# Kernel optimization log

Measured on AMD Instinct MI355X. Metric: run time of the kernel, lower is better.

Reference implementation:

```python
import jax, jax.numpy as jnp
import numpy as np

HEADS = 8
DIM_HEAD = 64
SCALE = DIM_HEAD ** (-0.5)


def setup_inputs() -> dict:
    key = jax.random.key(0)
    k1, k2, k3 = jax.random.split(key, 3)
    b, dim, w = 8, 256, 2048
    hidden = HEADS * DIM_HEAD  # 512
    x = jax.random.normal(k1, (b, dim, w), dtype=jnp.float32)
    # Conv1d kernel-size-1 weights collapse to matrices; scale like torch init
    w_qkv = jax.random.normal(k2, (3 * hidden, dim), dtype=jnp.float32) * (1.0 / np.sqrt(dim))
    w_out = jax.random.normal(k3, (dim, hidden), dtype=jnp.float32) * (1.0 / np.sqrt(hidden))
    b_out = jnp.zeros((dim,), dtype=jnp.float32)
    return {"x": x, "w_qkv": w_qkv, "w_out": w_out, "b_out": b_out}


def reference(x, w_qkv, w_out, b_out):
    b, c, w = x.shape
    h, dh = HEADS, DIM_HEAD
    # 1x1 conv == matmul over channel dim: [3*hidden, dim] x [b, dim, w] -> [b, 3*hidden, w]
    qkv = jnp.einsum('od,bdw->bow', w_qkv, x)
    q, k, v = jnp.split(qkv, 3, axis=1)
    # 'b (h c) x -> b h c x'
    q = q.reshape(b, h, dh, w) * SCALE
    k = k.reshape(b, h, dh, w)
    v = v.reshape(b, h, dh, w)
    sim = jnp.einsum('bhdi,bhdj->bhij', q, k)          # [b, h, w, w]
    sim = sim - jax.lax.stop_gradient(sim.max(axis=-1, keepdims=True))
    attn = jax.nn.softmax(sim, axis=-1)
    out = jnp.einsum('bhij,bhdj->bhid', attn, v)        # [b, h, w, dh]
    # 'b h x c -> b (h c) x'
    out = out.transpose(0, 1, 3, 2).reshape(b, h * dh, w)
    # output 1x1 conv with bias
    return jnp.einsum('oc,bcw->bow', w_out, out) + b_out[None, :, None]
```

## Files before the change

### kernel.cpp

```cpp
#include <hip/hip_runtime.h>
#include <hip/hip_bf16.h>

typedef __bf16 bf16x8 __attribute__((ext_vector_type(8)));
typedef float f32x4 __attribute__((ext_vector_type(4)));
typedef float f32x16 __attribute__((ext_vector_type(16)));
typedef unsigned u32x4 __attribute__((ext_vector_type(4)));

#define MFMA16x16(a, b, c) __builtin_amdgcn_mfma_f32_16x16x32_bf16((a), (b), (c), 0, 0, 0)
#define MFMA32x32(a, b, c) __builtin_amdgcn_mfma_f32_32x32x16_bf16((a), (b), (c), 0, 0, 0)

namespace {
constexpr int BATCH = 8;
constexpr int DIMC  = 256;
constexpr int WLEN  = 2048;
constexpr int DH    = 64;
constexpr int HID   = 512;
constexpr float QSCALE = 0.125f * 1.44269504088896340736f;

constexpr size_t OFF_WQKV = 0;
constexpr size_t OFF_WOUT = 786432;
constexpr size_t OFF_XT   = 1048576;
constexpr size_t OFF_QKT  = 9437184;
constexpr size_t OFF_V    = 42991616;
constexpr size_t OFF_AT   = 59768832;
}

__device__ inline unsigned cvt_pk_bf16(float a, float b) {
  unsigned r;
  asm("v_cvt_pk_bf16_f32 %0, %1, %2" : "=v"(r) : "v"(a), "v"(b));
  return r;
}

__device__ inline void permswap(unsigned &a, unsigned &b) {
  asm("v_permlane32_swap_b32 %0, %1" : "+v"(a), "+v"(b));
}

__device__ inline u32x4 gload16(const void* p) {
  u32x4 r;
  asm volatile("global_load_dwordx4 %0, %1, off" : "=v"(r) : "v"(p));
  return r;
}
__device__ inline void vmwait0() {
  asm volatile("s_waitcnt vmcnt(0)" ::: "memory");
  __builtin_amdgcn_sched_barrier(0);
}

union U4 { unsigned u[4]; bf16x8 v; };

__device__ inline float softmax_half(const f32x16 st, bf16x8 &pfa, bf16x8 &pfb) {
  float e[16];
#pragma unroll
  for (int r = 0; r < 16; ++r) e[r] = __builtin_amdgcn_exp2f(st[r]);
  float t0 = (e[0] + e[1]) + (e[2] + e[3]);
  float t1 = (e[4] + e[5]) + (e[6] + e[7]);
  float t2 = (e[8] + e[9]) + (e[10] + e[11]);
  float t3 = (e[12] + e[13]) + (e[14] + e[15]);
  float rs = (t0 + t1) + (t2 + t3);
  unsigned w[8];
#pragma unroll
  for (int q = 0; q < 8; ++q) w[q] = cvt_pk_bf16(e[2 * q], e[2 * q + 1]);
  unsigned a0 = w[0], a1 = w[1], a2 = w[2], a3 = w[3];
  permswap(a0, a2);
  permswap(a1, a3);
  U4 ua; ua.u[0] = a0; ua.u[1] = a1; ua.u[2] = a2; ua.u[3] = a3;
  pfa = ua.v;
  unsigned b0 = w[4], b1 = w[5], b2 = w[6], b3 = w[7];
  permswap(b0, b2);
  permswap(b1, b3);
  U4 ub; ub.u[0] = b0; ub.u[1] = b1; ub.u[2] = b2; ub.u[3] = b3;
  pfb = ub.v;
  return rs;
}

__global__ __launch_bounds__(256) void prep_weights(
    const float* __restrict__ wqkv, const float* __restrict__ wout,
    __hip_bfloat16* __restrict__ wqkv_bf, __hip_bfloat16* __restrict__ wout_bf) {
  int i = blockIdx.x * 256 + threadIdx.x;
  if (i < 1536 * 256) wqkv_bf[i] = __float2bfloat16(wqkv[i]);
  if (i < 256 * 512)  wout_bf[i] = __float2bfloat16(wout[i]);
}

__global__ __launch_bounds__(256) void transpose_x(
    const float* __restrict__ x, __hip_bfloat16* __restrict__ xT) {
  __shared__ float t[64][65];
  int b = blockIdx.z;
  int d0 = blockIdx.y * 64, w0 = blockIdx.x * 64;
  int tid = threadIdx.x;
  const float* xb = x + (size_t)b * DIMC * WLEN;
#pragma unroll
  for (int r = 0; r < 16; ++r) {
    int dd = r * 4 + (tid >> 6);
    int ww = tid & 63;
    t[dd][ww] = xb[(size_t)(d0 + dd) * WLEN + w0 + ww];
  }
  __syncthreads();
  __hip_bfloat16* xTb = xT + (size_t)b * WLEN * DIMC;
#pragma unroll
  for (int r = 0; r < 16; ++r) {
    int ww = r * 4 + (tid >> 6);
    int dd = tid & 63;
    xTb[(size_t)(w0 + ww) * DIMC + d0 + dd] = __float2bfloat16(t[dd][ww]);
  }
}

__global__ __launch_bounds__(256) void qkv_gemm(
    const __hip_bfloat16* __restrict__ wqkv_bf,
    const __hip_bfloat16* __restrict__ xT,
    __hip_bfloat16* __restrict__ qkT, __hip_bfloat16* __restrict__ vbuf) {
  int b = blockIdx.z;
  int o0 = blockIdx.y * 128, w0 = blockIdx.x * 128;
  int tid = threadIdx.x;
  int wid = tid >> 6, lane = tid & 63;
  int il = lane & 31, hi = lane >> 5;
  int wo = (wid >> 1) * 64;
  int ww = (wid & 1) * 64;

  __shared__ __align__(16) char lds_raw[36864];
  __hip_bfloat16* Al = reinterpret_cast<__hip_bfloat16*>(lds_raw);
  __hip_bfloat16* Bl = Al + 2 * 128 * 36;

  const __hip_bfloat16* xb = xT + (size_t)b * WLEN * DIMC;

  const int srow = tid >> 2;
  const int scol = (tid & 3) * 8;
  const __hip_bfloat16* asrc = wqkv_bf + (size_t)(o0 + srow) * DIMC + scol;
  const __hip_bfloat16* bsrc = xb + (size_t)(w0 + srow) * DIMC + scol;

  u32x4 ga0, ga1, gb0, gb1;
  auto stage_load = [&](int k0) {
    ga0 = gload16(asrc + k0);
    ga1 = gload16(asrc + 64 * DIMC + k0);
    gb0 = gload16(bsrc + k0);
    gb1 = gload16(bsrc + 64 * DIMC + k0);
  };
  auto stage_write = [&](int bf) {
    vmwait0();
    *reinterpret_cast<u32x4*>(Al + (bf * 128 + srow) * 36 + scol)      = ga0;
    *reinterpret_cast<u32x4*>(Al + (bf * 128 + srow + 64) * 36 + scol) = ga1;
    *reinterpret_cast<u32x4*>(Bl + (bf * 128 + srow) * 36 + scol)      = gb0;
    *reinterpret_cast<u32x4*>(Bl + (bf * 128 + srow + 64) * 36 + scol) = gb1;
  };

  f32x16 acc[2][2];
#pragma unroll
  for (int ta = 0; ta < 2; ++ta)
#pragma unroll
    for (int tb = 0; tb < 2; ++tb)
#pragma unroll
      for (int r = 0; r < 16; ++r) acc[ta][tb][r] = 0.f;

  auto compute = [&](int cur) {
    bf16x8 af[2][2], bfr[2][2];
#pragma unroll
    for (int ta = 0; ta < 2; ++ta)
#pragma unroll
      for (int kk = 0; kk < 2; ++kk) {
        af[ta][kk] = *reinterpret_cast<const bf16x8*>(
            Al + (cur * 128 + wo + ta * 32 + il) * 36 + kk * 16 + hi * 8);
        bfr[ta][kk] = *reinterpret_cast<const bf16x8*>(
            Bl + (cur * 128 + ww + ta * 32 + il) * 36 + kk * 16 + hi * 8);
      }
    __builtin_amdgcn_s_setprio(1);
#pragma unroll
    for (int kk = 0; kk < 2; ++kk)
#pragma unroll
      for (int ta = 0; ta < 2; ++ta)
#pragma unroll
        for (int tb = 0; tb < 2; ++tb)
          acc[ta][tb] = MFMA32x32(af[ta][kk], bfr[tb][kk], acc[ta][tb]);
    __builtin_amdgcn_s_setprio(0);
  };

  stage_load(0);
  stage_write(0);
  __syncthreads();
#pragma unroll 1
  for (int t = 0; t < 7; ++t) {
    stage_load((t + 1) * 32);
    compute(t & 1);
    stage_write((t + 1) & 1);
    __syncthreads();
  }
  compute(1);
  __syncthreads();

  if (o0 < 1024) {
    float scale = (o0 < 512) ? QSCALE : 1.0f;
    __hip_bfloat16* bw = reinterpret_cast<__hip_bfloat16*>(lds_raw);
#pragma unroll
    for (int ta = 0; ta < 2; ++ta)
#pragma unroll
      for (int tb = 0; tb < 2; ++tb)
#pragma unroll
        for (int q = 0; q < 8; ++q) {
          int dl = ((2 * q) & 3) + 8 * (q >> 1) + 4 * hi;
          int row = ww + tb * 32 + il;
          int col = wo + ta * 32 + dl;
          unsigned pk = cvt_pk_bf16(acc[ta][tb][2 * q] * scale,
                                    acc[ta][tb][2 * q + 1] * scale);
          *reinterpret_cast<unsigned*>(bw + row * 136 + col) = pk;
        }
    __syncthreads();
    __hip_bfloat16* outq = qkT + (size_t)b * WLEN * 1024;
#pragma unroll
    for (int it = 0; it < 8; ++it) {
      int row = it * 16 + (tid >> 4);
      int c = (tid & 15) * 8;
      bf16x8 v = *reinterpret_cast<const bf16x8*>(bw + row * 136 + c);
      *reinterpret_cast<bf16x8*>(outq + (size_t)(w0 + row) * 1024 + o0 + c) = v;
    }
  } else {
    __hip_bfloat16* bo = reinterpret_cast<__hip_bfloat16*>(lds_raw);
#pragma unroll
    for (int ta = 0; ta < 2; ++ta)
#pragma unroll
      for (int tb = 0; tb < 2; ++tb)
#pragma unroll
        for (int r = 0; r < 16; ++r) {
          int orow = wo + ta * 32 + (r & 3) + 8 * (r >> 2) + 4 * hi;
          int wcol = ww + tb * 32 + il;
          bo[orow * 136 + wcol] = __float2bfloat16(acc[ta][tb][r]);
        }
    __syncthreads();
    __hip_bfloat16* outv = vbuf + (size_t)b * HID * WLEN;
#pragma unroll
    for (int it = 0; it < 8; ++it) {
      int orow = it * 16 + (tid >> 4);
      int c = (tid & 15) * 8;
      bf16x8 v = *reinterpret_cast<const bf16x8*>(bo + orow * 136 + c);
      *reinterpret_cast<bf16x8*>(outv + (size_t)(o0 - 1024 + orow) * WLEN + w0 + c) = v;
    }
  }
}

__global__ __launch_bounds__(256) void attn_kernel(
    const __hip_bfloat16* __restrict__ qkT,
    const __hip_bfloat16* __restrict__ vbuf,
    __hip_bfloat16* __restrict__ attnT) {
  int f = blockIdx.x;
  int xcd = f & 7, slot = f >> 3;
  int b = slot >> 4;
  int h = xcd;
  int xb = slot & 15;
  int tid = threadIdx.x, wid = tid >> 6, lane = tid & 63;
  int il = lane & 31, hi = lane >> 5;
  int i0w = xb * 128 + wid * 32;

  const __hip_bfloat16* qk_b = qkT + (size_t)b * WLEN * 1024;
  const __hip_bfloat16* vb = vbuf + (size_t)b * HID * WLEN + (size_t)h * DH * WLEN;

  __shared__ __align__(16) __hip_bfloat16 Kl[2][64][72];
  __shared__ __align__(16) __hip_bfloat16 Vl[2][64][72];

  bf16x8 qf[4];
  {
    const __hip_bfloat16* qrow = qk_b + (size_t)(i0w + il) * 1024 + h * 64 + hi * 8;
#pragma unroll
    for (int s = 0; s < 4; ++s)
      qf[s] = *reinterpret_cast<const bf16x8*>(qrow + s * 16);
  }

  f32x16 oacc0, oacc1;
#pragma unroll
  for (int r = 0; r < 16; ++r) { oacc0[r] = 0.f; oacc1[r] = 0.f; }
  float l_lane = 0.f;

  const int srow = tid >> 3;
  const int scol = (tid & 7) * 8;
  const __hip_bfloat16* ksrc = qk_b + 512 + h * 64 + scol;
  const __hip_bfloat16* vsrc = vb + scol;

  u32x4 gk0, gk1, gv0, gv1;
  auto stage_load = [&](int j0) {
    gk0 = gload16(ksrc + (size_t)(j0 + srow) * 1024);
    gk1 = gload16(ksrc + (size_t)(j0 + srow + 32) * 1024);
    gv0 = gload16(vsrc + (size_t)srow * WLEN + j0);
    gv1 = gload16(vsrc + (size_t)(srow + 32) * WLEN + j0);
  };
  auto stage_write = [&](int bf) {
    vmwait0();
    *reinterpret_cast<u32x4*>(&Kl[bf][srow][scol])      = gk0;
    *reinterpret_cast<u32x4*>(&Kl[bf][srow + 32][scol]) = gk1;
    *reinterpret_cast<u32x4*>(&Vl[bf][srow][scol])      = gv0;
    *reinterpret_cast<u32x4*>(&Vl[bf][srow + 32][scol]) = gv1;
  };

  auto compute = [&](int cur) {
    f32x16 st0, st1;
#pragma unroll
    for (int r = 0; r < 16; ++r) { st0[r] = 0.f; st1[r] = 0.f; }
    __builtin_amdgcn_s_setprio(1);
#pragma unroll
    for (int s = 0; s < 4; ++s)
      st0 = MFMA32x32(*reinterpret_cast<const bf16x8*>(&Kl[cur][il][s * 16 + hi * 8]),
                      qf[s], st0);
#pragma unroll
    for (int s = 0; s < 4; ++s)
      st1 = MFMA32x32(*reinterpret_cast<const bf16x8*>(&Kl[cur][il + 32][s * 16 + hi * 8]),
                      qf[s], st1);
    __builtin_amdgcn_s_setprio(0);

    bf16x8 p0, p1, p2, p3;
    l_lane += softmax_half(st0, p0, p1);
    l_lane += softmax_half(st1, p2, p3);

    __builtin_amdgcn_s_setprio(1);
    oacc0 = MFMA32x32(*reinterpret_cast<const bf16x8*>(&Vl[cur][il][hi * 8]),      p0, oacc0);
    oacc1 = MFMA32x32(*reinterpret_cast<const bf16x8*>(&Vl[cur][il + 32][hi * 8]), p0, oacc1);
    oacc0 = MFMA32x32(*reinterpret_cast<const bf16x8*>(&Vl[cur][il][16 + hi * 8]),      p1, oacc0);
    oacc1 = MFMA32x32(*reinterpret_cast<const bf16x8*>(&Vl[cur][il + 32][16 + hi * 8]), p1, oacc1);
    oacc0 = MFMA32x32(*reinterpret_cast<const bf16x8*>(&Vl[cur][il][32 + hi * 8]),      p2, oacc0);
    oacc1 = MFMA32x32(*reinterpret_cast<const bf16x8*>(&Vl[cur][il + 32][32 + hi * 8]), p2, oacc1);
    oacc0 = MFMA32x32(*reinterpret_cast<const bf16x8*>(&Vl[cur][il][48 + hi * 8]),      p3, oacc0);
    oacc1 = MFMA32x32(*reinterpret_cast<const bf16x8*>(&Vl[cur][il + 32][48 + hi * 8]), p3, oacc1);
    __builtin_amdgcn_s_setprio(0);
  };

  stage_load(0);
  stage_write(0);
  __syncthreads();

  constexpr int NT = WLEN / 64;
#pragma unroll 1
  for (int t = 0; t < NT - 1; ++t) {
    stage_load((t + 1) * 64);
    compute(t & 1);
    stage_write((t + 1) & 1);
    __syncthreads();
  }
  compute((NT - 1) & 1);
  __syncthreads();

  float l = l_lane + __shfl_xor(l_lane, 32);
  __hip_bfloat16* olds = &Kl[0][0][0];
  float rl = 1.0f / l;
#pragma unroll
  for (int q = 0; q < 8; ++q) {
    int dl = ((2 * q) & 3) + 8 * (q >> 1) + 4 * hi;
    unsigned pk0 = cvt_pk_bf16(oacc0[2 * q] * rl, oacc0[2 * q + 1] * rl);
    unsigned pk1 = cvt_pk_bf16(oacc1[2 * q] * rl, oacc1[2 * q + 1] * rl);
    *reinterpret_cast<unsigned*>(olds + (wid * 32 + il) * 72 + dl)      = pk0;
    *reinterpret_cast<unsigned*>(olds + (wid * 32 + il) * 72 + 32 + dl) = pk1;
  }
  __hip_bfloat16* ob = attnT + (size_t)b * WLEN * HID + h * 64;
  int dcol = (lane & 7) * 8;
#pragma unroll
  for (int it = 0; it < 4; ++it) {
    int ir = it * 8 + (lane >> 3);
    bf16x8 vrow = *reinterpret_cast<const bf16x8*>(olds + (wid * 32 + ir) * 72 + dcol);
    *reinterpret_cast<bf16x8*>(ob + (size_t)(i0w + ir) * HID + dcol) = vrow;
  }
}

__global__ __launch_bounds__(256) void out_proj(
    const __hip_bfloat16* __restrict__ attnT,
    const __hip_bfloat16* __restrict__ wout_bf,
    const float* __restrict__ b_out, float* __restrict__ out) {
  int b = blockIdx.z;
  int o0 = blockIdx.y * 128, w0 = blockIdx.x * 64;
  int tid = threadIdx.x;
  int wid = tid >> 6, lane = tid & 63;
  int il = lane & 31, hi = lane >> 5;
  int wo = (wid >> 1) * 64;
  int ww = (wid & 1) * 32;

  __shared__ __align__(16) __hip_bfloat16 Al[2][128][36];
  __shared__ __align__(16) __hip_bfloat16 Bl[2][64][36];

  const __hip_bfloat16* at_b = attnT + (size_t)b * WLEN * HID;

  const int srow = tid >> 2;
  const int scol = (tid & 3) * 8;
  const __hip_bfloat16* asrc = wout_bf + (size_t)(o0 + srow) * HID + scol;
  const __hip_bfloat16* bsrc = at_b + (size_t)(w0 + srow) * HID + scol;

  u32x4 ga0, ga1, gb0;
  auto stage_load = [&](int k0) {
    ga0 = gload16(asrc + k0);
    ga1 = gload16(asrc + 64 * HID + k0);
    gb0 = gload16(bsrc + k0);
  };
  auto stage_write = [&](int bf) {
    vmwait0();
    *reinterpret_cast<u32x4*>(&Al[bf][srow][scol])      = ga0;
    *reinterpret_cast<u32x4*>(&Al[bf][srow + 64][scol]) = ga1;
    *reinterpret_cast<u32x4*>(&Bl[bf][srow][scol])      = gb0;
  };

  f32x16 acc[2];
#pragma unroll
  for (int ta = 0; ta < 2; ++ta)
#pragma unroll
    for (int r = 0; r < 16; ++r) acc[ta][r] = 0.f;

  auto compute = [&](int cur) {
    bf16x8 af[2][2], bfr[2];
#pragma unroll
    for (int kk = 0; kk < 2; ++kk) {
      bfr[kk] = *reinterpret_cast<const bf16x8*>(&Bl[cur][ww + il][kk * 16 + hi * 8]);
#pragma unroll
      for (int ta = 0; ta < 2; ++ta)
        af[ta][kk] = *reinterpret_cast<const bf16x8*>(
            &Al[cur][wo + ta * 32 + il][kk * 16 + hi * 8]);
    }
    __builtin_amdgcn_s_setprio(1);
#pragma unroll
    for (int kk = 0; kk < 2; ++kk)
#pragma unroll
      for (int ta = 0; ta < 2; ++ta)
        acc[ta] = MFMA32x32(af[ta][kk], bfr[kk], acc[ta]);
    __builtin_amdgcn_s_setprio(0);
  };

  stage_load(0);
  stage_write(0);
  __syncthreads();
#pragma unroll 1
  for (int t = 0; t < 15; ++t) {
    stage_load((t + 1) * 32);
    compute(t & 1);
    stage_write((t + 1) & 1);
    __syncthreads();
  }
  compute(1);

  float* outb = out + (size_t)b * DIMC * WLEN;
#pragma unroll
  for (int ta = 0; ta < 2; ++ta)
#pragma unroll
    for (int r = 0; r < 16; ++r) {
      int og = o0 + wo + ta * 32 + (r & 3) + 8 * (r >> 2) + 4 * hi;
      int wg = w0 + ww + il;
      outb[(size_t)og * WLEN + wg] = acc[ta][r] + b_out[og];
    }
}

extern "C" void kernel_launch(void* const* d_in, const int* in_sizes, int n_in,
                              void* d_out, int out_size, void* d_ws, size_t ws_size,
                              hipStream_t stream) {
  const float* x    = (const float*)d_in[0];
  const float* wqkv = (const float*)d_in[1];
  const float* wout = (const float*)d_in[2];
  const float* bout = (const float*)d_in[3];
  float* out = (float*)d_out;
  char* ws = (char*)d_ws;

  __hip_bfloat16* wqkv_bf = (__hip_bfloat16*)(ws + OFF_WQKV);
  __hip_bfloat16* wout_bf = (__hip_bfloat16*)(ws + OFF_WOUT);
  __hip_bfloat16* xT      = (__hip_bfloat16*)(ws + OFF_XT);
  __hip_bfloat16* qkT     = (__hip_bfloat16*)(ws + OFF_QKT);
  __hip_bfloat16* vbuf    = (__hip_bfloat16*)(ws + OFF_V);
  __hip_bfloat16* attnT   = (__hip_bfloat16*)(ws + OFF_AT);

  prep_weights<<<dim3(1536), dim3(256), 0, stream>>>(wqkv, wout, wqkv_bf, wout_bf);
  transpose_x<<<dim3(WLEN / 64, DIMC / 64, BATCH), dim3(256), 0, stream>>>(x, xT);
  qkv_gemm<<<dim3(WLEN / 128, 1536 / 128, BATCH), dim3(256), 0, stream>>>(wqkv_bf, xT, qkT, vbuf);
  attn_kernel<<<dim3(1024), dim3(256), 0, stream>>>(qkT, vbuf, attnT);
  out_proj<<<dim3(WLEN / 64, DIMC / 128, BATCH), dim3(256), 0, stream>>>(attnT, wout_bf, bout, out);
}
```

Before: 190.7 us.

## Process 64 query rows per wave in attention to reuse K/V fragments

Each wave now handles two 32-row query tiles (A and B), so every K and V fragment read from LDS feeds four MFMAs instead of two. The grid is halved to 512 blocks of 256 query rows each. Shared memory becomes a padded raw 72KB buffer, which limits occupancy to about two blocks per CU. The goal is to cut LDS traffic and K/V global loads per unit of work, at the cost of higher register pressure and fewer blocks to spread across the CUs.

```diff
diff --git a/kernel.cpp b/kernel.cpp
--- a/kernel.cpp
+++ b/kernel.cpp
@@ -238,32 +238,37 @@
     const __hip_bfloat16* __restrict__ vbuf,
     __hip_bfloat16* __restrict__ attnT) {
   int f = blockIdx.x;
-  int xcd = f & 7, slot = f >> 3;
-  int b = slot >> 4;
-  int h = xcd;
-  int xb = slot & 15;
+  int h = f & 7, slot = f >> 3;
+  int b = slot >> 3;
+  int xb = slot & 7;
   int tid = threadIdx.x, wid = tid >> 6, lane = tid & 63;
   int il = lane & 31, hi = lane >> 5;
-  int i0w = xb * 128 + wid * 32;
+  int i0w = xb * 256 + wid * 64;
 
   const __hip_bfloat16* qk_b = qkT + (size_t)b * WLEN * 1024;
   const __hip_bfloat16* vb = vbuf + (size_t)b * HID * WLEN + (size_t)h * DH * WLEN;
 
-  __shared__ __align__(16) __hip_bfloat16 Kl[2][64][72];
-  __shared__ __align__(16) __hip_bfloat16 Vl[2][64][72];
-
-  bf16x8 qf[4];
+  __shared__ __align__(16) char araw[73728];
+  __hip_bfloat16* Kl = reinterpret_cast<__hip_bfloat16*>(araw);
+  __hip_bfloat16* Vl = Kl + 2 * 64 * 72;
+
+  bf16x8 qfA[4], qfB[4];
   {
-    const __hip_bfloat16* qrow = qk_b + (size_t)(i0w + il) * 1024 + h * 64 + hi * 8;
-#pragma unroll
-    for (int s = 0; s < 4; ++s)
-      qf[s] = *reinterpret_cast<const bf16x8*>(qrow + s * 16);
-  }
-
-  f32x16 oacc0, oacc1;
-#pragma unroll
-  for (int r = 0; r < 16; ++r) { oacc0[r] = 0.f; oacc1[r] = 0.f; }
-  float l_lane = 0.f;
+    const __hip_bfloat16* qa = qk_b + (size_t)(i0w + il) * 1024 + h * 64 + hi * 8;
+#pragma unroll
+    for (int s = 0; s < 4; ++s) {
+      qfA[s] = *reinterpret_cast<const bf16x8*>(qa + s * 16);
+      qfB[s] = *reinterpret_cast<const bf16x8*>(qa + 32 * 1024 + s * 16);
+    }
+  }
+
+  f32x16 oA0, oA1, oB0, oB1;
+  f32x16 fzero;
+#pragma unroll
+  for (int r = 0; r < 16; ++r) {
+    oA0[r] = 0.f; oA1[r] = 0.f; oB0[r] = 0.f; oB1[r] = 0.f; fzero[r] = 0.f;
+  }
+  float lA = 0.f, lB = 0.f;
 
   const int srow = tid >> 3;
   const int scol = (tid & 7) * 8;
@@ -279,40 +284,52 @@
   };
   auto stage_write = [&](int bf) {
     vmwait0();
-    *reinterpret_cast<u32x4*>(&Kl[bf][srow][scol])      = gk0;
-    *reinterpret_cast<u32x4*>(&Kl[bf][srow + 32][scol]) = gk1;
-    *reinterpret_cast<u32x4*>(&Vl[bf][srow][scol])      = gv0;
-    *reinterpret_cast<u32x4*>(&Vl[bf][srow + 32][scol]) = gv1;
+    *reinterpret_cast<u32x4*>(Kl + (bf * 64 + srow) * 72 + scol)      = gk0;
+    *reinterpret_cast<u32x4*>(Kl + (bf * 64 + srow + 32) * 72 + scol) = gk1;
+    *reinterpret_cast<u32x4*>(Vl + (bf * 64 + srow) * 72 + scol)      = gv0;
+    *reinterpret_cast<u32x4*>(Vl + (bf * 64 + srow + 32) * 72 + scol) = gv1;
   };
 
   auto compute = [&](int cur) {
-    f32x16 st0, st1;
-#pragma unroll
-    for (int r = 0; r < 16; ++r) { st0[r] = 0.f; st1[r] = 0.f; }
+    f32x16 sA0, sA1, sB0, sB1;
+    const __hip_bfloat16* kb = Kl + (size_t)cur * 64 * 72 + hi * 8;
     __builtin_amdgcn_s_setprio(1);
-#pragma unroll
-    for (int s = 0; s < 4; ++s)
-      st0 = MFMA32x32(*reinterpret_cast<const bf16x8*>(&Kl[cur][il][s * 16 + hi * 8]),
-                      qf[s], st0);
-#pragma unroll
-    for (int s = 0; s < 4; ++s)
-      st1 = MFMA32x32(*reinterpret_cast<const bf16x8*>(&Kl[cur][il + 32][s * 16 + hi * 8]),
-                      qf[s], st1);
+    {
+      bf16x8 k0 = *reinterpret_cast<const bf16x8*>(kb + il * 72);
+      bf16x8 k1 = *reinterpret_cast<const bf16x8*>(kb + (il + 32) * 72);
+      sA0 = MFMA32x32(k0, qfA[0], fzero);
+      sA1 = MFMA32x32(k1, qfA[0], fzero);
+      sB0 = MFMA32x32(k0, qfB[0], fzero);
+      sB1 = MFMA32x32(k1, qfB[0], fzero);
+    }
+#pragma unroll
+    for (int s = 1; s < 4; ++s) {
+      bf16x8 k0 = *reinterpret_cast<const bf16x8*>(kb + il * 72 + s * 16);
+      bf16x8 k1 = *reinterpret_cast<const bf16x8*>(kb + (il + 32) * 72 + s * 16);
+      sA0 = MFMA32x32(k0, qfA[s], sA0);
+      sA1 = MFMA32x32(k1, qfA[s], sA1);
+      sB0 = MFMA32x32(k0, qfB[s], sB0);
+      sB1 = MFMA32x32(k1, qfB[s], sB1);
+    }
     __builtin_amdgcn_s_setprio(0);
 
-    bf16x8 p0, p1, p2, p3;
-    l_lane += softmax_half(st0, p0, p1);
-    l_lane += softmax_half(st1, p2, p3);
-
+    bf16x8 pA[4], pB[4];
+    lA += softmax_half(sA0, pA[0], pA[1]);
+    lA += softmax_half(sA1, pA[2], pA[3]);
+    lB += softmax_half(sB0, pB[0], pB[1]);
+    lB += softmax_half(sB1, pB[2], pB[3]);
+
+    const __hip_bfloat16* vbl = Vl + (size_t)cur * 64 * 72 + hi * 8;
     __builtin_amdgcn_s_setprio(1);
-    oacc0 = MFMA32x32(*reinterpret_cast<const bf16x8*>(&Vl[cur][il][hi * 8]),      p0, oacc0);
-    oacc1 = MFMA32x32(*reinterpret_cast<const bf16x8*>(&Vl[cur][il + 32][hi * 8]), p0, oacc1);
-    oacc0 = MFMA32x32(*reinterpret_cast<const bf16x8*>(&Vl[cur][il][16 + hi * 8]),      p1, oacc0);
-    oacc1 = MFMA32x32(*reinterpret_cast<const bf16x8*>(&Vl[cur][il + 32][16 + hi * 8]), p1, oacc1);
-    oacc0 = MFMA32x32(*reinterpret_cast<const bf16x8*>(&Vl[cur][il][32 + hi * 8]),      p2, oacc0);
-    oacc1 = MFMA32x32(*reinterpret_cast<const bf16x8*>(&Vl[cur][il + 32][32 + hi * 8]), p2, oacc1);
-    oacc0 = MFMA32x32(*reinterpret_cast<const bf16x8*>(&Vl[cur][il][48 + hi * 8]),      p3, oacc0);
-    oacc1 = MFMA32x32(*reinterpret_cast<const bf16x8*>(&Vl[cur][il + 32][48 + hi * 8]), p3, oacc1);
+#pragma unroll
+    for (int ks = 0; ks < 4; ++ks) {
+      bf16x8 v0 = *reinterpret_cast<const bf16x8*>(vbl + il * 72 + ks * 16);
+      bf16x8 v1 = *reinterpret_cast<const bf16x8*>(vbl + (il + 32) * 72 + ks * 16);
+      oA0 = MFMA32x32(v0, pA[ks], oA0);
+      oA1 = MFMA32x32(v1, pA[ks], oA1);
+      oB0 = MFMA32x32(v0, pB[ks], oB0);
+      oB1 = MFMA32x32(v1, pB[ks], oB1);
+    }
     __builtin_amdgcn_s_setprio(0);
   };
 
@@ -331,24 +348,30 @@
   compute((NT - 1) & 1);
   __syncthreads();
 
-  float l = l_lane + __shfl_xor(l_lane, 32);
-  __hip_bfloat16* olds = &Kl[0][0][0];
-  float rl = 1.0f / l;
+  lA += __shfl_xor(lA, 32);
+  lB += __shfl_xor(lB, 32);
+  float rlA = 1.0f / lA, rlB = 1.0f / lB;
+  __hip_bfloat16* olds = reinterpret_cast<__hip_bfloat16*>(araw);
+  int rowA = wid * 64 + il, rowB = rowA + 32;
 #pragma unroll
   for (int q = 0; q < 8; ++q) {
     int dl = ((2 * q) & 3) + 8 * (q >> 1) + 4 * hi;
-    unsigned pk0 = cvt_pk_bf16(oacc0[2 * q] * rl, oacc0[2 * q + 1] * rl);
-    unsigned pk1 = cvt_pk_bf16(oacc1[2 * q] * rl, oacc1[2 * q + 1] * rl);
-    *reinterpret_cast<unsigned*>(olds + (wid * 32 + il) * 72 + dl)      = pk0;
-    *reinterpret_cast<unsigned*>(olds + (wid * 32 + il) * 72 + 32 + dl) = pk1;
+    *reinterpret_cast<unsigned*>(olds + rowA * 72 + dl) =
+        cvt_pk_bf16(oA0[2 * q] * rlA, oA0[2 * q + 1] * rlA);
+    *reinterpret_cast<unsigned*>(olds + rowA * 72 + 32 + dl) =
+        cvt_pk_bf16(oA1[2 * q] * rlA, oA1[2 * q + 1] * rlA);
+    *reinterpret_cast<unsigned*>(olds + rowB * 72 + dl) =
+        cvt_pk_bf16(oB0[2 * q] * rlB, oB0[2 * q + 1] * rlB);
+    *reinterpret_cast<unsigned*>(olds + rowB * 72 + 32 + dl) =
+        cvt_pk_bf16(oB1[2 * q] * rlB, oB1[2 * q + 1] * rlB);
   }
   __hip_bfloat16* ob = attnT + (size_t)b * WLEN * HID + h * 64;
   int dcol = (lane & 7) * 8;
 #pragma unroll
-  for (int it = 0; it < 4; ++it) {
-    int ir = it * 8 + (lane >> 3);
-    bf16x8 vrow = *reinterpret_cast<const bf16x8*>(olds + (wid * 32 + ir) * 72 + dcol);
-    *reinterpret_cast<bf16x8*>(ob + (size_t)(i0w + ir) * HID + dcol) = vrow;
+  for (int it = 0; it < 8; ++it) {
+    int ir = wid * 64 + it * 8 + (lane >> 3);
+    bf16x8 vrow = *reinterpret_cast<const bf16x8*>(olds + ir * 72 + dcol);
+    *reinterpret_cast<bf16x8*>(ob + (size_t)(xb * 256 + ir) * HID + dcol) = vrow;
   }
 }
 
@@ -455,6 +478,6 @@
   prep_weights<<<dim3(1536), dim3(256), 0, stream>>>(wqkv, wout, wqkv_bf, wout_bf);
   transpose_x<<<dim3(WLEN / 64, DIMC / 64, BATCH), dim3(256), 0, stream>>>(x, xT);
   qkv_gemm<<<dim3(WLEN / 128, 1536 / 128, BATCH), dim3(256), 0, stream>>>(wqkv_bf, xT, qkT, vbuf);
-  attn_kernel<<<dim3(1024), dim3(256), 0, stream>>>(qkT, vbuf, attnT);
+  attn_kernel<<<dim3(512), dim3(256), 0, stream>>>(qkT, vbuf, attnT);
   out_proj<<<dim3(WLEN / 64, DIMC / 128, BATCH), dim3(256), 0, stream>>>(attnT, wout_bf, bout, out);
 }
```

Result: slower. 205.2 us (+7.6%).
